# Optimization experiments

Measured on AMD Instinct MI355X. Metric: run time of the kernel, lower is better.

## Reference

```python
import jax, jax.numpy as jnp
import numpy as np

B, S, D_IN, Z, D_OUT = 4, 2048, 4096, 1024, 4096
LN_EPS = 1e-5


def _ln(h, g, b):
    # LayerNorm over last axis (matches nn.LayerNorm(z_size))
    m = jnp.mean(h, axis=-1, keepdims=True)
    v = jnp.var(h, axis=-1, keepdims=True)
    return (h - m) * jax.lax.rsqrt(v + LN_EPS) * g + b


def setup_inputs() -> dict:
    key = jax.random.key(0)
    ks = jax.random.split(key, 8)
    s = 0.02  # init_weights uniform range
    return {
        "x": jax.random.normal(ks[0], (B, S, D_IN), jnp.float32),
        "epsilon": jax.random.normal(ks[1], (B, S, Z), jnp.float32),
        "W1": jax.random.uniform(ks[2], (Z, D_IN), jnp.float32, -s, s),
        "b1": jnp.zeros((Z,), jnp.float32),
        "g1": jnp.ones((Z,), jnp.float32),
        "be1": jnp.zeros((Z,), jnp.float32),
        "W2": jax.random.uniform(ks[3], (Z, Z), jnp.float32, -s, s),
        "b2": jnp.zeros((Z,), jnp.float32),
        "g2": jnp.ones((Z,), jnp.float32),
        "be2": jnp.zeros((Z,), jnp.float32),
        "Wmu": jax.random.uniform(ks[4], (Z, Z), jnp.float32, -s, s),
        "bmu": jnp.zeros((Z,), jnp.float32),
        "Wls": jax.random.uniform(ks[5], (Z, Z), jnp.float32, -s, s),
        "bls": jnp.zeros((Z,), jnp.float32),
        "Wzw": jax.random.uniform(ks[6], (D_OUT, D_OUT + Z), jnp.float32, -s, s),
        "bzw": jnp.zeros((D_OUT,), jnp.float32),
    }


def reference(x, epsilon, W1, b1, g1, be1, W2, b2, g2, be2,
              Wmu, bmu, Wls, bls, Wzw, bzw):
    # fc: Linear -> LayerNorm -> Tanh, twice
    h = jnp.tanh(_ln(jnp.einsum('bsd,zd->bsz', x, W1) + b1, g1, be1))
    h = jnp.tanh(_ln(jnp.einsum('bsz,yz->bsy', h, W2) + b2, g2, be2))
    mu = jnp.einsum('bsz,yz->bsy', h, Wmu) + bmu
    logsigma = jnp.einsum('bsz,yz->bsy', h, Wls) + bls
    std = jnp.exp(0.5 * logsigma)
    z = epsilon * std + mu                    # reparameterization
    z = jnp.concatenate([z, x], axis=2)       # [B,S,Z+D_IN]
    out = jnp.einsum('bsc,oc->bso', jnp.tanh(z), Wzw) + bzw
    return (out, mu, std)
```

## Files before the change

### kernel.cpp

```cpp
#include <hip/hip_runtime.h>
#include <cstdint>

typedef unsigned short u16;
typedef __bf16 bf16x8 __attribute__((ext_vector_type(8)));
typedef float f32x4 __attribute__((ext_vector_type(4)));

#define M_TOT 8192
#define D_IN  4096
#define Z_DIM 1024
#define D_OUT 4096
#define K_CAT 5120

struct alignas(8) u16x4 { u16 x, y, z, w; };

__device__ __forceinline__ u16 to_bf16(float f) {
    union { float f; uint32_t u; } v; v.f = f;
    uint32_t u = v.u;
    uint32_t r = (u + 0x7FFFu + ((u >> 16) & 1u)) >> 16;
    return (u16)r;
}

__device__ __forceinline__ void async_load16(const void* g, void* l) {
    __builtin_amdgcn_global_load_lds(
        (const __attribute__((address_space(1))) void*)g,
        (__attribute__((address_space(3))) void*)l,
        16, 0, 0);
}

#define BAR() do { asm volatile("" ::: "memory"); \
                   __builtin_amdgcn_s_barrier(); \
                   asm volatile("" ::: "memory"); } while (0)


#define STAGE_A(buf, h, kt_) do { if ((kt_) < nt) {                            \
    const u16* g_ = Ag + (long long)(h) * hstep + ((long long)(kt_) << 6);     \
    async_load16(g_,      &lds16[(buf) * 32768 + (h) * 8192        + wave * 512]); \
    async_load16(g_ + 32, &lds16[(buf) * 32768 + (h) * 8192 + 4096 + wave * 512]); \
  } } while (0)

#define STAGE_B(buf, h, kt_) do { if ((kt_) < nt) {                            \
    const u16* g_ = Bg + (long long)(h) * hstep + ((long long)(kt_) << 6);     \
    async_load16(g_,      &lds16[16384 + (buf) * 32768 + (h) * 8192        + wave * 512]); \
    async_load16(g_ + 32, &lds16[16384 + (buf) * 32768 + (h) * 8192 + 4096 + wave * 512]); \
  } } while (0)

#define LOAD_AF(buf, mbase)                                                    \
    _Pragma("unroll")                                                          \
    for (int mi_ = 0; mi_ < 4; ++mi_) {                                        \
      _Pragma("unroll")                                                        \
      for (int ks_ = 0; ks_ < 2; ++ks_)                                        \
        af[mi_][ks_] = *(const bf16x8*)&lds16[(buf) * 32768 + a_rd             \
                                              + ks_ * 4096 + ((mbase) + mi_) * 512]; \
    }

#define LOAD_B(dst, buf, nbase)                                                \
    _Pragma("unroll")                                                          \
    for (int ni_ = 0; ni_ < 2; ++ni_) {                                        \
      _Pragma("unroll")                                                        \
      for (int ks_ = 0; ks_ < 2; ++ks_)                                        \
        dst[ni_][ks_] = *(const bf16x8*)&lds16[(buf) * 32768 + b_rd            \
                                               + ks_ * 4096 + ((nbase) + ni_) * 512]; \
    }

#define MMA_Q(bfx, mo, no) do {                                                \
    __builtin_amdgcn_s_setprio(1);                                             \
    _Pragma("unroll")                                                          \
    for (int mi_ = 0; mi_ < 4; ++mi_) {                                        \
      _Pragma("unroll")                                                        \
      for (int ni_ = 0; ni_ < 2; ++ni_) {                                      \
        _Pragma("unroll")                                                      \
        for (int ks_ = 0; ks_ < 2; ++ks_)                                      \
          acc[(mo) + mi_][(no) + ni_] = __builtin_amdgcn_mfma_f32_16x16x32_bf16( \
              af[mi_][ks_], bfx[ni_][ks_], acc[(mo) + mi_][(no) + ni_], 0, 0, 0); \
      }                                                                        \
    }                                                                          \
    __builtin_amdgcn_s_setprio(0);                                             \
  } while (0)

#define TILE(b, kt_) do {                                                      \
    LOAD_AF(b, 0);                                                             \
    STAGE_A((b) ^ 1, 0, (kt_) + 1);                                            \
    BAR();                                                                     \
    MMA_Q(bf0, 0, 0);                                                          \
    BAR();                                                                     \
    LOAD_B(bf1, b, 2);                                                         \
    STAGE_A((b) ^ 1, 1, (kt_) + 1);                                            \
    BAR();                                                                     \
    MMA_Q(bf1, 0, 2);                                                          \
    BAR();                                                                     \
    LOAD_AF(b, 4);                                                             \
    STAGE_B(b, 0, (kt_) + 2);                                                  \
    BAR();                                                                     \
    MMA_Q(bf0, 4, 0);                                                          \
    BAR();                                                                     \
    STAGE_B(b, 1, (kt_) + 2);                                                  \
    if ((kt_) + 2 < nt) { asm volatile("s_waitcnt vmcnt(4)" ::: "memory"); }   \
    else                { asm volatile("s_waitcnt vmcnt(0)" ::: "memory"); }   \
    BAR();                                                                     \
    LOAD_B(bf0, (b) ^ 1, 0);                                                   \
    MMA_Q(bf1, 4, 2);                                                          \
    BAR();                                                                     \
  } while (0)

template <bool EXPLS>
__global__ __launch_bounds__(512)
void gemm256(const u16* __restrict__ A,
             const u16* __restrict__ Bw0, const u16* __restrict__ Bw1,
             const float* __restrict__ bias0, const float* __restrict__ bias1,
             float* __restrict__ C0, float* __restrict__ C1,
             int M, int N, int K)
{
    const u16*   Bw   = blockIdx.z ? Bw1   : Bw0;
    const float* bias = blockIdx.z ? bias1 : bias0;
    float*       C    = blockIdx.z ? C1    : C0;

    __shared__ u16 lds16[65536];

    const int tid  = threadIdx.x;
    const int wave = tid >> 6;
    const int lane = tid & 63;
    const int fr   = lane & 15;
    const int fq   = lane >> 4;
    const int wm   = (wave >> 2) * 128;
    const int wn   = (wave & 3) * 64;

    const int nwg  = (int)(gridDim.x * gridDim.y);
    const int bid0 = (int)(blockIdx.y * gridDim.x + blockIdx.x);
    const int bid  = (bid0 & 7) * (nwg >> 3) + (bid0 >> 3);
    const int n0   = (bid % (int)gridDim.x) * 256;
    const int m0   = (bid / (int)gridDim.x) * 256;

    const int nt = K >> 6;

    const int csrc = (tid & 3) ^ ((tid >> 4) & 2);
    const u16* Ag = A  + (long long)(m0 + (tid >> 2)) * K + csrc * 8;
    const u16* Bg = Bw + (long long)(n0 + (tid >> 2)) * K + csrc * 8;
    const long long hstep = 128LL * K;

    const int swz  = (fq * 8) ^ ((fr & 8) << 1);
    const int a_rd = (wave >> 2) * 8192 + fr * 32 + swz;
    const int b_rd = 16384 + ((wave & 3) >> 1) * 8192
                   + ((wave & 1) * 64 + fr) * 32 + swz;

    f32x4 acc[8][4] = {};
    bf16x8 af[4][2], bf0[2][2], bf1[2][2];

    STAGE_B(0, 0, 0);
    STAGE_B(0, 1, 0);
    STAGE_A(0, 0, 0);
    STAGE_A(0, 1, 0);
    STAGE_B(1, 0, 1);
    STAGE_B(1, 1, 1);
    asm volatile("s_waitcnt vmcnt(4)" ::: "memory");
    BAR();
    LOAD_B(bf0, 0, 0);

    #pragma unroll 1
    for (int kt = 0; kt < nt; kt += 2) {
        TILE(0, kt);
        TILE(1, kt + 1);
    }

    #pragma unroll
    for (int ni = 0; ni < 4; ++ni) {
        const int col = n0 + wn + ni * 16 + fr;
        const float bv = bias[col];
        #pragma unroll
        for (int mi = 0; mi < 8; ++mi) {
            const int row = m0 + wm + mi * 16 + fq * 4;
            float* cp = C + (long long)row * N + col;
            #pragma unroll
            for (int r = 0; r < 4; ++r) {
                float v = acc[mi][ni][r] + bv;
                if constexpr (EXPLS) { if (blockIdx.z) v = expf(0.5f * v); }
                cp[(long long)r * N] = v;
            }
        }
    }
}

#undef STAGE_A
#undef STAGE_B
#undef LOAD_AF
#undef LOAD_B
#undef MMA_Q
#undef TILE


#define STAGE_A1(buf, h, kt_) do { if ((kt_) < nt) {                           \
    const u16* g_ = Ag + (long long)(h) * hstep + ((long long)(kt_) << 6);     \
    async_load16(g_,      &lds16[(buf) * 24576 + (h) * 8192        + wave * 512]); \
    async_load16(g_ + 32, &lds16[(buf) * 24576 + (h) * 8192 + 4096 + wave * 512]); \
  } } while (0)

#define STAGE_B1(buf, kt_) do { if ((kt_) < nt) {                              \
    const u16* g_ = Bg + ((long long)(kt_) << 6);                              \
    async_load16(g_,      &lds16[(buf) * 24576 + 16384        + wave * 512]);  \
    async_load16(g_ + 32, &lds16[(buf) * 24576 + 16384 + 4096 + wave * 512]);  \
  } } while (0)

#define LOAD_AF1(buf, mbase)                                                   \
    _Pragma("unroll")                                                          \
    for (int mi_ = 0; mi_ < 4; ++mi_) {                                        \
      _Pragma("unroll")                                                        \
      for (int ks_ = 0; ks_ < 2; ++ks_)                                        \
        af[mi_][ks_] = *(const bf16x8*)&lds16[(buf) * 24576 + a_rd             \
                                              + ks_ * 4096 + ((mbase) + mi_) * 512]; \
    }

#define LOAD_BF1(dst, buf)                                                     \
    _Pragma("unroll")                                                          \
    for (int ni_ = 0; ni_ < 2; ++ni_) {                                        \
      _Pragma("unroll")                                                        \
      for (int ks_ = 0; ks_ < 2; ++ks_)                                        \
        dst[ni_][ks_] = *(const bf16x8*)&lds16[(buf) * 24576 + b_rd            \
                                               + ks_ * 4096 + ni_ * 512];      \
    }

#define MMA_H(bfx, mo) do {                                                    \
    __builtin_amdgcn_s_setprio(1);                                             \
    _Pragma("unroll")                                                          \
    for (int mi_ = 0; mi_ < 4; ++mi_) {                                        \
      _Pragma("unroll")                                                        \
      for (int ni_ = 0; ni_ < 2; ++ni_) {                                      \
        _Pragma("unroll")                                                      \
        for (int ks_ = 0; ks_ < 2; ++ks_)                                      \
          acc[(mo) + mi_][ni_] = __builtin_amdgcn_mfma_f32_16x16x32_bf16(      \
              af[mi_][ks_], bfx[ni_][ks_], acc[(mo) + mi_][ni_], 0, 0, 0);     \
      }                                                                        \
    }                                                                          \
    __builtin_amdgcn_s_setprio(0);                                             \
  } while (0)

#define TILE1(b, kt_, bfCur, bfNxt) do {                                       \
                                     \
    LOAD_AF1(b, 0);                                                            \
    STAGE_A1((b) ^ 1, 0, (kt_) + 1);                                           \
    BAR();                                                                     \
    MMA_H(bfCur, 0);                                                           \
    BAR();                                                                     \
         \
    LOAD_AF1(b, 4);                                                            \
    STAGE_A1((b) ^ 1, 1, (kt_) + 1);                                           \
    STAGE_B1(b, (kt_) + 2);                                                    \
    if ((kt_) + 2 < nt) { asm volatile("s_waitcnt vmcnt(2)" ::: "memory"); }   \
    else                { asm volatile("s_waitcnt vmcnt(0)" ::: "memory"); }   \
    BAR();                                                                     \
    LOAD_BF1(bfNxt, (b) ^ 1);                                                  \
    MMA_H(bfCur, 4);                                                           \
    BAR();                                                                     \
  } while (0)

__global__ __launch_bounds__(512)
void gemm128n(const u16* __restrict__ A, const u16* __restrict__ Bw,
              const float* __restrict__ bias, float* __restrict__ C,
              int M, int N, int K)
{
    __shared__ u16 lds16[49152];

    const int tid  = threadIdx.x;
    const int wave = tid >> 6;
    const int lane = tid & 63;
    const int fr   = lane & 15;
    const int fq   = lane >> 4;
    const int wm   = (wave >> 2) * 128;
    const int wn   = (wave & 3) * 32;

    const int nwg  = (int)(gridDim.x * gridDim.y);
    const int bid0 = (int)(blockIdx.y * gridDim.x + blockIdx.x);
    const int bid  = (bid0 & 7) * (nwg >> 3) + (bid0 >> 3);
    const int n0   = (bid % (int)gridDim.x) * 128;
    const int m0   = (bid / (int)gridDim.x) * 256;

    const int nt = K >> 6;

    const int csrc = (tid & 3) ^ ((tid >> 4) & 2);
    const u16* Ag = A  + (long long)(m0 + (tid >> 2)) * K + csrc * 8;
    const u16* Bg = Bw + (long long)(n0 + (tid >> 2)) * K + csrc * 8;
    const long long hstep = 128LL * K;

    const int swz  = (fq * 8) ^ ((fr & 8) << 1);
    const int a_rd = (wave >> 2) * 8192 + fr * 32 + swz;
    const int b_rd = 16384 + ((wave & 3) * 32 + fr) * 32 + swz;

    f32x4 acc[8][2] = {};
    bf16x8 af[4][2], bfA[2][2], bfB[2][2];

    STAGE_B1(0, 0);
    STAGE_A1(0, 0, 0);
    STAGE_A1(0, 1, 0);
    STAGE_B1(1, 1);
    asm volatile("s_waitcnt vmcnt(2)" ::: "memory");
    BAR();
    LOAD_BF1(bfA, 0);

    #pragma unroll 1
    for (int kt = 0; kt < nt; kt += 2) {
        TILE1(0, kt,     bfA, bfB);
        TILE1(1, kt + 1, bfB, bfA);
    }

    #pragma unroll
    for (int ni = 0; ni < 2; ++ni) {
        const int col = n0 + wn + ni * 16 + fr;
        const float bv = bias[col];
        #pragma unroll
        for (int mi = 0; mi < 8; ++mi) {
            const int row = m0 + wm + mi * 16 + fq * 4;
            float* cp = C + (long long)row * N + col;
            #pragma unroll
            for (int r = 0; r < 4; ++r)
                cp[(long long)r * N] = acc[mi][ni][r] + bv;
        }
    }
}

#undef STAGE_A1
#undef STAGE_B1
#undef LOAD_AF1
#undef LOAD_BF1
#undef MMA_H
#undef TILE1

__global__ __launch_bounds__(256)
void ln_tanh_kernel(const float* __restrict__ in, const float* __restrict__ g,
                    const float* __restrict__ be, u16* __restrict__ out)
{
    const int row = blockIdx.x;
    const int t = threadIdx.x;
    const float4 v = ((const float4*)(in + (long long)row * 1024))[t];
    float s  = v.x + v.y + v.z + v.w;
    float s2 = v.x * v.x + v.y * v.y + v.z * v.z + v.w * v.w;
    #pragma unroll
    for (int off = 32; off > 0; off >>= 1) {
        s  += __shfl_down(s,  off);
        s2 += __shfl_down(s2, off);
    }
    __shared__ float red[8];
    if ((t & 63) == 0) { red[t >> 6] = s; red[4 + (t >> 6)] = s2; }
    __syncthreads();
    s  = red[0] + red[1] + red[2] + red[3];
    s2 = red[4] + red[5] + red[6] + red[7];
    const float mean = s * (1.0f / 1024.0f);
    const float inv  = rsqrtf(s2 * (1.0f / 1024.0f) - mean * mean + 1e-5f);
    const float4 gg = ((const float4*)g)[t];
    const float4 bb = ((const float4*)be)[t];
    u16x4 o;
    o.x = to_bf16(tanhf((v.x - mean) * inv * gg.x + bb.x));
    o.y = to_bf16(tanhf((v.y - mean) * inv * gg.y + bb.y));
    o.z = to_bf16(tanhf((v.z - mean) * inv * gg.z + bb.z));
    o.w = to_bf16(tanhf((v.w - mean) * inv * gg.w + bb.w));
    ((u16x4*)(out + (long long)row * 1024))[t] = o;
}

__global__ __launch_bounds__(256)
void prep_x_kernel(const float* __restrict__ x, u16* __restrict__ xb,
                   u16* __restrict__ zc)
{
    const long long i = (long long)blockIdx.x * 256 + threadIdx.x;
    const float4 v = ((const float4*)x)[i];
    u16x4 b;
    b.x = to_bf16(v.x); b.y = to_bf16(v.y); b.z = to_bf16(v.z); b.w = to_bf16(v.w);
    ((u16x4*)xb)[i] = b;
    const long long flat = i * 4;
    const long long row = flat >> 12;
    const int col = (int)(flat & 4095);
    u16x4 tq;
    tq.x = to_bf16(tanhf(v.x)); tq.y = to_bf16(tanhf(v.y));
    tq.z = to_bf16(tanhf(v.z)); tq.w = to_bf16(tanhf(v.w));
    *(u16x4*)(zc + row * (long long)K_CAT + 1024 + col) = tq;
}

__global__ __launch_bounds__(256)
void reparam_kernel(const float* __restrict__ mu, const float* __restrict__ stdv,
                    const float* __restrict__ eps, u16* __restrict__ zc)
{
    const long long row = blockIdx.x;
    const int c = threadIdx.x * 4;
    const long long idx = row * 1024 + c;
    const float4 m = *(const float4*)(mu + idx);
    const float4 sd = *(const float4*)(stdv + idx);
    const float4 e = *(const float4*)(eps + idx);
    u16x4 t;
    t.x = to_bf16(tanhf(e.x * sd.x + m.x));
    t.y = to_bf16(tanhf(e.y * sd.y + m.y));
    t.z = to_bf16(tanhf(e.z * sd.z + m.z));
    t.w = to_bf16(tanhf(e.w * sd.w + m.w));
    *(u16x4*)(zc + row * (long long)K_CAT + c) = t;
}

__global__ __launch_bounds__(256)
void cvt_kernel(const float* __restrict__ src, u16* __restrict__ dst, long long n4)
{
    const long long i = (long long)blockIdx.x * 256 + threadIdx.x;
    if (i >= n4) return;
    const float4 v = ((const float4*)src)[i];
    u16x4 b;
    b.x = to_bf16(v.x); b.y = to_bf16(v.y); b.z = to_bf16(v.z); b.w = to_bf16(v.w);
    ((u16x4*)dst)[i] = b;
}

__global__ __launch_bounds__(256)
void cvt4_kernel(const float* __restrict__ s0, u16* __restrict__ d0,
                 const float* __restrict__ s1, u16* __restrict__ d1,
                 const float* __restrict__ s2, u16* __restrict__ d2,
                 const float* __restrict__ s3, u16* __restrict__ d3)
{
    long long i = (long long)blockIdx.x * 256 + threadIdx.x;
    const float* s; u16* d;
    if (i < 1048576)      { s = s0; d = d0; }
    else if (i < 1310720) { s = s1; d = d1; i -= 1048576; }
    else if (i < 1572864) { s = s2; d = d2; i -= 1310720; }
    else                  { s = s3; d = d3; i -= 1572864; }
    const float4 v = ((const float4*)s)[i];
    u16x4 b;
    b.x = to_bf16(v.x); b.y = to_bf16(v.y); b.z = to_bf16(v.z); b.w = to_bf16(v.w);
    ((u16x4*)d)[i] = b;
}

extern "C" void kernel_launch(void* const* d_in, const int* in_sizes, int n_in,
                              void* d_out, int out_size, void* d_ws, size_t ws_size,
                              hipStream_t stream)
{
    const float* x   = (const float*)d_in[0];
    const float* eps = (const float*)d_in[1];
    const float* W1  = (const float*)d_in[2];
    const float* b1  = (const float*)d_in[3];
    const float* g1  = (const float*)d_in[4];
    const float* be1 = (const float*)d_in[5];
    const float* W2  = (const float*)d_in[6];
    const float* b2  = (const float*)d_in[7];
    const float* g2  = (const float*)d_in[8];
    const float* be2 = (const float*)d_in[9];
    const float* Wmu = (const float*)d_in[10];
    const float* bmu = (const float*)d_in[11];
    const float* Wls = (const float*)d_in[12];
    const float* bls = (const float*)d_in[13];
    const float* Wzw = (const float*)d_in[14];
    const float* bzw = (const float*)d_in[15];

    float* out  = (float*)d_out;
    float* mu   = out + (long long)M_TOT * D_OUT;
    float* std_ = mu  + (long long)M_TOT * Z_DIM;

    char* ws = (char*)d_ws;
    u16*   xb   = (u16*)(ws);
    u16*   zc   = (u16*)(ws +  67108864);
    u16*   h1   = (u16*)(ws + 150994944);
    u16*   h2   = (u16*)(ws + 167772160);
    float* pre  = (float*)(ws + 184549376);
    u16*   W1b  = (u16*)(ws + 218103808);
    u16*   W2b  = (u16*)(ws + 226492416);
    u16*   Wmub = (u16*)(ws + 228589568);
    u16*   Wlsb = (u16*)(ws + 230686720);
    u16*   Wzwb = (u16*)(ws);

    cvt4_kernel<<<7168, 256, 0, stream>>>(W1, W1b, W2, W2b, Wmu, Wmub, Wls, Wlsb);

    prep_x_kernel<<<32768, 256, 0, stream>>>(x, xb, zc);

    gemm128n<<<dim3(8, 32, 1), 512, 0, stream>>>(xb, W1b, b1, pre,
                                                 M_TOT, Z_DIM, D_IN);
    ln_tanh_kernel<<<8192, 256, 0, stream>>>(pre, g1, be1, h1);

    cvt_kernel<<<20480, 256, 0, stream>>>(Wzw, Wzwb, 5242880);

    gemm128n<<<dim3(8, 32, 1), 512, 0, stream>>>(h1, W2b, b2, pre,
                                                 M_TOT, Z_DIM, Z_DIM);
    ln_tanh_kernel<<<8192, 256, 0, stream>>>(pre, g2, be2, h2);

    gemm256<true><<<dim3(4, 32, 2), 512, 0, stream>>>(h2, Wmub, Wlsb, bmu, bls,
                                                      mu, std_,
                                                      M_TOT, Z_DIM, Z_DIM);

    reparam_kernel<<<8192, 256, 0, stream>>>(mu, std_, eps, zc);

    gemm256<false><<<dim3(16, 32, 1), 512, 0, stream>>>(zc, Wzwb, Wzwb, bzw, bzw,
                                                        out, out,
                                                        M_TOT, D_OUT, K_CAT);
}
```

Measured before the change: 877.2 us.

## Fuse mu/logsigma GEMMs with reparameterization epilogue and use fast tanh

Adds a gemm_heads kernel that computes the mu and logsigma projections together in one pass over the shared A tiles. Its epilogue applies exp, the reparameterization and tanh, and writes bf16 into the concat buffer, so the separate reparam kernel and its reread of mu/std are removed. It also replaces tanhf with an exp/rcp based fast_tanh in the LN and prep kernels. The trade-offs are higher register pressure from two accumulator sets, uncoalesced strided epilogue stores, and slightly lower tanh accuracy.

```diff
diff --git a/kernel.cpp b/kernel.cpp
--- a/kernel.cpp
+++ b/kernel.cpp
@@ -18,6 +18,11 @@
     uint32_t u = v.u;
     uint32_t r = (u + 0x7FFFu + ((u >> 16) & 1u)) >> 16;
     return (u16)r;
+}
+
+__device__ __forceinline__ float fast_tanh(float x) {
+    const float e = __expf(2.0f * x);
+    return 1.0f - 2.0f * __builtin_amdgcn_rcpf(e + 1.0f);
 }
 
 __device__ __forceinline__ void async_load16(const void* g, void* l) {
@@ -102,18 +107,11 @@
     BAR();                                                                     \
   } while (0)
 
-template <bool EXPLS>
 __global__ __launch_bounds__(512)
-void gemm256(const u16* __restrict__ A,
-             const u16* __restrict__ Bw0, const u16* __restrict__ Bw1,
-             const float* __restrict__ bias0, const float* __restrict__ bias1,
-             float* __restrict__ C0, float* __restrict__ C1,
+void gemm256(const u16* __restrict__ A, const u16* __restrict__ Bw,
+             const float* __restrict__ bias, float* __restrict__ C,
              int M, int N, int K)
 {
-    const u16*   Bw   = blockIdx.z ? Bw1   : Bw0;
-    const float* bias = blockIdx.z ? bias1 : bias0;
-    float*       C    = blockIdx.z ? C1    : C0;
-
     __shared__ u16 lds16[65536];
 
     const int tid  = threadIdx.x;
@@ -170,11 +168,8 @@
             const int row = m0 + wm + mi * 16 + fq * 4;
             float* cp = C + (long long)row * N + col;
             #pragma unroll
-            for (int r = 0; r < 4; ++r) {
-                float v = acc[mi][ni][r] + bv;
-                if constexpr (EXPLS) { if (blockIdx.z) v = expf(0.5f * v); }
-                cp[(long long)r * N] = v;
-            }
+            for (int r = 0; r < 4; ++r)
+                cp[(long long)r * N] = acc[mi][ni][r] + bv;
         }
     }
 }
@@ -233,13 +228,11 @@
   } while (0)
 
 #define TILE1(b, kt_, bfCur, bfNxt) do {                                       \
-                                     \
     LOAD_AF1(b, 0);                                                            \
     STAGE_A1((b) ^ 1, 0, (kt_) + 1);                                           \
     BAR();                                                                     \
     MMA_H(bfCur, 0);                                                           \
     BAR();                                                                     \
-         \
     LOAD_AF1(b, 4);                                                            \
     STAGE_A1((b) ^ 1, 1, (kt_) + 1);                                           \
     STAGE_B1(b, (kt_) + 2);                                                    \
@@ -322,6 +315,158 @@
 #undef MMA_H
 #undef TILE1
 
+
+#define STAGE_AH(buf, h, kt_) do { if ((kt_) < nt) {                           \
+    const u16* g_ = Ag + (long long)(h) * hstep + ((long long)(kt_) << 6);     \
+    async_load16(g_,      &lds16[(buf) * 32768 + (h) * 8192        + wave * 512]); \
+    async_load16(g_ + 32, &lds16[(buf) * 32768 + (h) * 8192 + 4096 + wave * 512]); \
+  } } while (0)
+
+#define STAGE_BH(buf, bsel, kt_) do { if ((kt_) < nt) {                        \
+    const u16* g_ = ((bsel) ? Blsg : Bmug) + ((long long)(kt_) << 6);          \
+    async_load16(g_,      &lds16[(buf) * 32768 + 16384 + (bsel) * 8192        + wave * 512]); \
+    async_load16(g_ + 32, &lds16[(buf) * 32768 + 16384 + (bsel) * 8192 + 4096 + wave * 512]); \
+  } } while (0)
+
+#define LOAD_AFH(buf, mbase)                                                   \
+    _Pragma("unroll")                                                          \
+    for (int mi_ = 0; mi_ < 4; ++mi_) {                                        \
+      _Pragma("unroll")                                                        \
+      for (int ks_ = 0; ks_ < 2; ++ks_)                                        \
+        af[mi_][ks_] = *(const bf16x8*)&lds16[(buf) * 32768 + a_rd             \
+                                              + ks_ * 4096 + ((mbase) + mi_) * 512]; \
+    }
+
+#define LOAD_BH(dst, buf, bsel)                                                \
+    _Pragma("unroll")                                                          \
+    for (int ni_ = 0; ni_ < 2; ++ni_) {                                        \
+      _Pragma("unroll")                                                        \
+      for (int ks_ = 0; ks_ < 2; ++ks_)                                        \
+        dst[ni_][ks_] = *(const bf16x8*)&lds16[(buf) * 32768 + 16384           \
+                + (bsel) * 8192 + bh_rd + ks_ * 4096 + ni_ * 512];             \
+    }
+
+#define MMA_H2(accX, bfx, mo) do {                                             \
+    __builtin_amdgcn_s_setprio(1);                                             \
+    _Pragma("unroll")                                                          \
+    for (int mi_ = 0; mi_ < 4; ++mi_) {                                        \
+      _Pragma("unroll")                                                        \
+      for (int ni_ = 0; ni_ < 2; ++ni_) {                                      \
+        _Pragma("unroll")                                                      \
+        for (int ks_ = 0; ks_ < 2; ++ks_)                                      \
+          accX[(mo) + mi_][ni_] = __builtin_amdgcn_mfma_f32_16x16x32_bf16(     \
+              af[mi_][ks_], bfx[ni_][ks_], accX[(mo) + mi_][ni_], 0, 0, 0);    \
+      }                                                                        \
+    }                                                                          \
+    __builtin_amdgcn_s_setprio(0);                                             \
+  } while (0)
+
+#define TILE_H(b, kt_) do {                                                    \
+           \
+    LOAD_AFH(b, 0);                                                            \
+    LOAD_BH(bfMu, b, 0);                                                       \
+    LOAD_BH(bfLs, b, 1);                                                       \
+    STAGE_AH((b) ^ 1, 0, (kt_) + 1);                                           \
+    BAR();                                                                     \
+    MMA_H2(accMu, bfMu, 0);                                                    \
+    MMA_H2(accLs, bfLs, 0);                                                    \
+    BAR();                                                                     \
+           \
+    LOAD_AFH(b, 4);                                                            \
+    STAGE_AH((b) ^ 1, 1, (kt_) + 1);                                           \
+    STAGE_BH(b, 0, (kt_) + 2);                                                 \
+    STAGE_BH(b, 1, (kt_) + 2);                                                 \
+    if ((kt_) + 2 < nt) { asm volatile("s_waitcnt vmcnt(4)" ::: "memory"); }   \
+    else                { asm volatile("s_waitcnt vmcnt(0)" ::: "memory"); }   \
+    BAR();                                                                     \
+    MMA_H2(accMu, bfMu, 4);                                                    \
+    MMA_H2(accLs, bfLs, 4);                                                    \
+    BAR();                                                                     \
+  } while (0)
+
+__global__ __launch_bounds__(512)
+void gemm_heads(const u16* __restrict__ A,
+                const u16* __restrict__ Wmu, const u16* __restrict__ Wls,
+                const float* __restrict__ bmu, const float* __restrict__ bls,
+                const float* __restrict__ eps,
+                float* __restrict__ muO, float* __restrict__ stdO,
+                u16* __restrict__ zc, int K)
+{
+    __shared__ u16 lds16[65536];
+
+    const int tid  = threadIdx.x;
+    const int wave = tid >> 6;
+    const int lane = tid & 63;
+    const int fr   = lane & 15;
+    const int fq   = lane >> 4;
+    const int wm   = (wave >> 2) * 128;
+    const int wn   = (wave & 3) * 32;
+
+    const int nwg  = (int)(gridDim.x * gridDim.y);
+    const int bid0 = (int)(blockIdx.y * gridDim.x + blockIdx.x);
+    const int bid  = (bid0 & 7) * (nwg >> 3) + (bid0 >> 3);
+    const int n0   = (bid % (int)gridDim.x) * 128;
+    const int m0   = (bid / (int)gridDim.x) * 256;
+
+    const int nt = K >> 6;
+
+    const int csrc = (tid & 3) ^ ((tid >> 4) & 2);
+    const u16* Ag   = A   + (long long)(m0 + (tid >> 2)) * K + csrc * 8;
+    const u16* Bmug = Wmu + (long long)(n0 + (tid >> 2)) * K + csrc * 8;
+    const u16* Blsg = Wls + (long long)(n0 + (tid >> 2)) * K + csrc * 8;
+    const long long hstep = 128LL * K;
+
+    const int swz   = (fq * 8) ^ ((fr & 8) << 1);
+    const int a_rd  = (wave >> 2) * 8192 + fr * 32 + swz;
+    const int bh_rd = ((wave & 3) * 32 + fr) * 32 + swz;
+
+    f32x4 accMu[8][2] = {}, accLs[8][2] = {};
+    bf16x8 af[4][2], bfMu[2][2], bfLs[2][2];
+
+    STAGE_BH(0, 0, 0);
+    STAGE_BH(0, 1, 0);
+    STAGE_AH(0, 0, 0);
+    STAGE_AH(0, 1, 0);
+    STAGE_BH(1, 0, 1);
+    STAGE_BH(1, 1, 1);
+    asm volatile("s_waitcnt vmcnt(4)" ::: "memory");
+    BAR();
+
+    #pragma unroll 1
+    for (int kt = 0; kt < nt; kt += 2) {
+        TILE_H(0, kt);
+        TILE_H(1, kt + 1);
+    }
+
+    #pragma unroll
+    for (int ni = 0; ni < 2; ++ni) {
+        const int col = n0 + wn + ni * 16 + fr;
+        const float bmu_v = bmu[col];
+        const float bls_v = bls[col];
+        #pragma unroll
+        for (int mi = 0; mi < 8; ++mi) {
+            const int row = m0 + wm + mi * 16 + fq * 4;
+            #pragma unroll
+            for (int r = 0; r < 4; ++r) {
+                const long long idx = (long long)(row + r) * 1024 + col;
+                const float muv = accMu[mi][ni][r] + bmu_v;
+                const float sdv = expf(0.5f * (accLs[mi][ni][r] + bls_v));
+                muO[idx]  = muv;
+                stdO[idx] = sdv;
+                const float z = eps[idx] * sdv + muv;
+                zc[(long long)(row + r) * K_CAT + col] = to_bf16(fast_tanh(z));
+            }
+        }
+    }
+}
+
+#undef STAGE_AH
+#undef STAGE_BH
+#undef LOAD_AFH
+#undef LOAD_BH
+#undef MMA_H2
+#undef TILE_H
+
 __global__ __launch_bounds__(256)
 void ln_tanh_kernel(const float* __restrict__ in, const float* __restrict__ g,
                     const float* __restrict__ be, u16* __restrict__ out)
@@ -346,10 +491,10 @@
     const float4 gg = ((const float4*)g)[t];
     const float4 bb = ((const float4*)be)[t];
     u16x4 o;
-    o.x = to_bf16(tanhf((v.x - mean) * inv * gg.x + bb.x));
-    o.y = to_bf16(tanhf((v.y - mean) * inv * gg.y + bb.y));
-    o.z = to_bf16(tanhf((v.z - mean) * inv * gg.z + bb.z));
-    o.w = to_bf16(tanhf((v.w - mean) * inv * gg.w + bb.w));
+    o.x = to_bf16(fast_tanh((v.x - mean) * inv * gg.x + bb.x));
+    o.y = to_bf16(fast_tanh((v.y - mean) * inv * gg.y + bb.y));
+    o.z = to_bf16(fast_tanh((v.z - mean) * inv * gg.z + bb.z));
+    o.w = to_bf16(fast_tanh((v.w - mean) * inv * gg.w + bb.w));
     ((u16x4*)(out + (long long)row * 1024))[t] = o;
 }
 
@@ -366,27 +511,9 @@
     const long long row = flat >> 12;
     const int col = (int)(flat & 4095);
     u16x4 tq;
-    tq.x = to_bf16(tanhf(v.x)); tq.y = to_bf16(tanhf(v.y));
-    tq.z = to_bf16(tanhf(v.z)); tq.w = to_bf16(tanhf(v.w));
+    tq.x = to_bf16(fast_tanh(v.x)); tq.y = to_bf16(fast_tanh(v.y));
+    tq.z = to_bf16(fast_tanh(v.z)); tq.w = to_bf16(fast_tanh(v.w));
     *(u16x4*)(zc + row * (long long)K_CAT + 1024 + col) = tq;
-}
-
-__global__ __launch_bounds__(256)
-void reparam_kernel(const float* __restrict__ mu, const float* __restrict__ stdv,
-                    const float* __restrict__ eps, u16* __restrict__ zc)
-{
-    const long long row = blockIdx.x;
-    const int c = threadIdx.x * 4;
-    const long long idx = row * 1024 + c;
-    const float4 m = *(const float4*)(mu + idx);
-    const float4 sd = *(const float4*)(stdv + idx);
-    const float4 e = *(const float4*)(eps + idx);
-    u16x4 t;
-    t.x = to_bf16(tanhf(e.x * sd.x + m.x));
-    t.y = to_bf16(tanhf(e.y * sd.y + m.y));
-    t.z = to_bf16(tanhf(e.z * sd.z + m.z));
-    t.w = to_bf16(tanhf(e.w * sd.w + m.w));
-    *(u16x4*)(zc + row * (long long)K_CAT + c) = t;
 }
 
 __global__ __launch_bounds__(256)
@@ -469,13 +596,9 @@
                                                  M_TOT, Z_DIM, Z_DIM);
     ln_tanh_kernel<<<8192, 256, 0, stream>>>(pre, g2, be2, h2);
 
-    gemm256<true><<<dim3(4, 32, 2), 512, 0, stream>>>(h2, Wmub, Wlsb, bmu, bls,
-                                                      mu, std_,
-                                                      M_TOT, Z_DIM, Z_DIM);
-
-    reparam_kernel<<<8192, 256, 0, stream>>>(mu, std_, eps, zc);
-
-    gemm256<false><<<dim3(16, 32, 1), 512, 0, stream>>>(zc, Wzwb, Wzwb, bzw, bzw,
-                                                        out, out,
-                                                        M_TOT, D_OUT, K_CAT);
-}
+    gemm_heads<<<dim3(8, 32, 1), 512, 0, stream>>>(h2, Wmub, Wlsb, bmu, bls,
+                                                   eps, mu, std_, zc, Z_DIM);
+
+    gemm256<<<dim3(16, 32, 1), 512, 0, stream>>>(zc, Wzwb, bzw, out,
+                                                 M_TOT, D_OUT, K_CAT);
+}
```

Result: slower. 922.8 us (+5.2%).
